# Optimization experiments

Measured on AMD Instinct MI355X. Metric: run time of the kernel, lower is better.

## Reference

```python
import jax, jax.numpy as jnp
import numpy as np
import math

B, S, SD = 8, 256, 768            # batch, seq_len, sent_dim (roberta-base)
L, NH, DH, FF = 12, 12, 64, 3072  # bert layers, heads, head dim, ffn dim
K, D, HC, DPH = 5, 200, 4, 50     # gnn layers, concept_dim, gat heads, dim/head
NNT, NET = 4, 38                  # node / edge types
NN = 200                          # nodes per graph
N = B * NN                        # total nodes
E = 50000                         # edges (before self loops)
IE = 200                          # info-exchange MLP hidden dim
LN_EPS = 1e-12
BN_EPS = 1e-5

def _gelu(x):
    return jax.nn.gelu(x, approximate=False)

def _layer_norm(x, w, b):
    m = jnp.mean(x, -1, keepdims=True)
    v = jnp.mean(jnp.square(x - m), -1, keepdims=True)
    return (x - m) * jax.lax.rsqrt(v + LN_EPS) * w + b

def _bn_eval(x, w, b):
    # untrained BatchNorm1d in eval mode: running_mean=0, running_var=1
    return x * np.float32(1.0 / np.sqrt(1.0 + BN_EPS)) * w + b

def _segment_softmax(scores, seg, num_segments):
    smax = jax.ops.segment_max(scores, seg, num_segments=num_segments)
    ex = jnp.exp(scores - smax[seg])
    den = jax.ops.segment_sum(ex, seg, num_segments=num_segments)
    return ex / (den[seg] + 1e-16)

def setup_inputs():
    key = jax.random.key(0)
    ks = iter(jax.random.split(key, 64))
    def nrm(shape, scale=0.02):
        return jax.random.normal(next(ks), shape, jnp.float32) * scale
    z = lambda s: jnp.zeros(s, jnp.float32)
    o = lambda s: jnp.ones(s, jnp.float32)
    return {
        'hidden_states': nrm((B, S, SD), 1.0),
        'attention_mask': z((B, 1, 1, S)),
        '_X': nrm((N, D), 1.0),
        '_node_feature_extra': nrm((N, D), 1.0),
        'qkv_w': nrm((L, 3, SD, SD)), 'qkv_b': z((L, 3, SD)),
        'attn_out_w': nrm((L, SD, SD)), 'attn_out_b': z((L, SD)),
        'ln1_w': o((L, SD)), 'ln1_b': z((L, SD)),
        'ffn_w1': nrm((L, SD, FF)), 'ffn_b1': z((L, FF)),
        'ffn_w2': nrm((L, FF, SD)), 'ffn_b2': z((L, SD)),
        'ln2_w': o((L, SD)), 'ln2_b': z((L, SD)),
        'ee_w1': nrm((NET + 1 + 2 * NNT, D)), 'ee_b1': z((D,)),
        'ee_bn_w': o((D,)), 'ee_bn_b': z((D,)),
        'ee_w2': nrm((D, D)), 'ee_b2': z((D,)),
        'gat_key_w': nrm((K, 3 * D, D)), 'gat_key_b': z((K, D)),
        'gat_msg_w': nrm((K, 3 * D, D)), 'gat_msg_b': z((K, D)),
        'gat_query_w': nrm((K, 2 * D, D)), 'gat_query_b': z((K, D)),
        'gat_mlp_w1': nrm((K, D, D)), 'gat_mlp_b1': z((K, D)),
        'gat_mlp_bn_w': o((K, D)), 'gat_mlp_bn_b': z((K, D)),
        'gat_mlp_w2': nrm((K, D, D)), 'gat_mlp_b2': z((K, D)),
        'ie_w1': nrm((SD + D, IE)), 'ie_b1': z((IE,)),
        'ie_w2': nrm((IE, SD + D)), 'ie_b2': z((SD + D,)),
        'edge_index': jax.random.randint(next(ks), (2, E), 0, N, dtype=jnp.int32),
        'edge_type': jax.random.randint(next(ks), (E,), 0, NET, dtype=jnp.int32),
        '_node_type': jax.random.randint(next(ks), (N,), 0, NNT, dtype=jnp.int32),
    }

def _forward(hidden_states, attention_mask, _X, _node_feature_extra,
             qkv_w, qkv_b, attn_out_w, attn_out_b, ln1_w, ln1_b,
             ffn_w1, ffn_b1, ffn_w2, ffn_b2, ln2_w, ln2_b,
             ee_w1, ee_b1, ee_bn_w, ee_bn_b, ee_w2, ee_b2,
             gat_key_w, gat_key_b, gat_msg_w, gat_msg_b, gat_query_w, gat_query_b,
             gat_mlp_w1, gat_mlp_b1, gat_mlp_bn_w, gat_mlp_bn_b, gat_mlp_w2, gat_mlp_b2,
             ie_w1, ie_b1, ie_w2, ie_b2,
             edge_index, edge_type, _node_type):
    hs = hidden_states
    dt = hs.dtype
    # ---- edge embeddings (shared edge_encoder => identical every gnn layer) ----
    loop = jnp.arange(N, dtype=edge_index.dtype)
    src = jnp.concatenate([edge_index[0], loop])   # [E+N] with self loops
    tgt = jnp.concatenate([edge_index[1], loop])
    edge_vec = jax.nn.one_hot(edge_type, NET + 1, dtype=dt)
    self_edge_vec = jnp.zeros((N, NET + 1), dt).at[:, NET].set(1.0)
    head_vec = jax.nn.one_hot(_node_type[edge_index[0]], NNT, dtype=dt)
    tail_vec = jax.nn.one_hot(_node_type[edge_index[1]], NNT, dtype=dt)
    self_vec = jax.nn.one_hot(_node_type, NNT, dtype=dt)
    feat = jnp.concatenate([
        jnp.concatenate([edge_vec, head_vec, tail_vec], 1),
        jnp.concatenate([self_edge_vec, self_vec, self_vec], 1)], 0)  # [E+N, 47]
    h = jax.nn.relu(_bn_eval(feat @ ee_w1 + ee_b1, ee_bn_w, ee_bn_b))
    edge_emb = h @ ee_w2 + ee_b2                                       # [E+N, D]
    deg_src = jax.ops.segment_sum(jnp.ones(src.shape, dt), src, num_segments=N)[src]
    scale_q = np.float32(1.0 / math.sqrt(DPH))
    scale_a = np.float32(1.0 / math.sqrt(DH))

    def gat_layer(Xc, g):
        x2 = jnp.concatenate([Xc, _node_feature_extra], 1)             # [N, 2D]
        x_i, x_j = x2[tgt], x2[src]                                    # tgt / src gathers
        key = (jnp.concatenate([x_i, edge_emb], 1) @ gat_key_w[g] + gat_key_b[g]).reshape(-1, HC, DPH)
        msg = (jnp.concatenate([x_j, edge_emb], 1) @ gat_msg_w[g] + gat_msg_b[g]).reshape(-1, HC, DPH)
        qry = (x_j @ gat_query_w[g] + gat_query_b[g]).reshape(-1, HC, DPH) * scale_q
        scores = jnp.sum(qry * key, -1)                                 # [E+N, HC]
        alpha = _segment_softmax(scores, src, N) * deg_src[:, None]     # grouped over src, degree-rescaled
        out = (msg * alpha[..., None]).reshape(-1, HC * DPH)
        aggr = jax.ops.segment_sum(out, tgt, num_segments=N)            # [N, D]
        hm = jax.nn.relu(_bn_eval(aggr @ gat_mlp_w1[g] + gat_mlp_b1[g], gat_mlp_bn_w[g], gat_mlp_bn_b[g]))
        return hm @ gat_mlp_w2[g] + gat_mlp_b2[g]

    Xc = _X
    for i in range(L):
        q = (hs @ qkv_w[i, 0] + qkv_b[i, 0]).reshape(B, S, NH, DH).transpose(0, 2, 1, 3)
        k = (hs @ qkv_w[i, 1] + qkv_b[i, 1]).reshape(B, S, NH, DH).transpose(0, 2, 1, 3)
        v = (hs @ qkv_w[i, 2] + qkv_b[i, 2]).reshape(B, S, NH, DH).transpose(0, 2, 1, 3)
        att = jax.nn.softmax(jnp.einsum('bhqd,bhkd->bhqk', q, k) * scale_a + attention_mask, -1)
        ctx = jnp.einsum('bhqk,bhkd->bhqd', att, v).transpose(0, 2, 1, 3).reshape(B, S, SD)
        attn = _layer_norm(ctx @ attn_out_w[i] + attn_out_b[i] + hs, ln1_w[i], ln1_b[i])
        inter = _gelu(attn @ ffn_w1[i] + ffn_b1[i])
        hs = _layer_norm(inter @ ffn_w2[i] + ffn_b2[i] + attn, ln2_w[i], ln2_b[i])
        if i >= L - K:
            g = i - L + K
            Xc = _gelu(gat_layer(Xc, g))
            Xv = Xc.reshape(B, NN, D)
            cf = jnp.concatenate([hs[:, 0, :], Xv[:, 0, :]], 1)         # [B, SD+D]
            cf = _gelu(cf @ ie_w1 + ie_b1) @ ie_w2 + ie_b2              # ie MLP (residual_ie=0)
            hs = hs.at[:, 0, :].set(cf[:, :SD])
            Xc = Xv.at[:, 0, :].set(cf[:, SD:]).reshape(N, D)
    return hs, Xc

def reference(hidden_states, attention_mask, _X, _node_feature_extra,
              qkv_w, qkv_b, attn_out_w, attn_out_b, ln1_w, ln1_b,
              ffn_w1, ffn_b1, ffn_w2, ffn_b2, ln2_w, ln2_b,
              ee_w1, ee_b1, ee_bn_w, ee_bn_b, ee_w2, ee_b2,
              gat_key_w, gat_key_b, gat_msg_w, gat_msg_b, gat_query_w, gat_query_b,
              gat_mlp_w1, gat_mlp_b1, gat_mlp_bn_w, gat_mlp_bn_b, gat_mlp_w2, gat_mlp_b2,
              ie_w1, ie_b1, ie_w2, ie_b2,
              edge_index, edge_type, _node_type):
    return _forward(hidden_states, attention_mask, _X, _node_feature_extra,
                    qkv_w, qkv_b, attn_out_w, attn_out_b, ln1_w, ln1_b,
                    ffn_w1, ffn_b1, ffn_w2, ffn_b2, ln2_w, ln2_b,
                    ee_w1, ee_b1, ee_bn_w, ee_bn_b, ee_w2, ee_b2,
                    gat_key_w, gat_key_b, gat_msg_w, gat_msg_b, gat_query_w, gat_query_b,
                    gat_mlp_w1, gat_mlp_b1, gat_mlp_bn_w, gat_mlp_bn_b, gat_mlp_w2, gat_mlp_b2,
                    ie_w1, ie_b1, ie_w2, ie_b2,
                    edge_index, edge_type, _node_type)
```

## Files before the change

kernel.cpp:

```cpp
#include <hip/hip_runtime.h>
#include <math.h>

namespace {
constexpr int CB = 8, CS = 256, CSD = 768, CL = 12, CNH = 12, CDH = 64, CFF = 3072;
constexpr int CK = 5, CD = 200, CHC = 4, CDPH = 50, CNNT = 4, CNET = 38;
constexpr int CNN = 200, CN = 1600, CE = 50000, CEN = 51600, CIE = 200;
constexpr int KP200 = 256, KP400 = 448;

constexpr long long OPK   = 0;
constexpr long long OATN  = OPK  + 3145728;
constexpr long long OXC   = OATN + 1572864;
constexpr long long OSC   = OXC  + 320000;
constexpr long long OSMX  = OSC  + 206400;
constexpr long long ODEN  = OSMX + 6400;
constexpr long long ODEG  = ODEN + 6400;
constexpr long long OAGG  = ODEG + 1600;
constexpr long long OQN   = OAGG + 320000;
constexpr long long OKN   = OQN  + 320000;
constexpr long long OMN   = OKN  + 320000;
constexpr long long OCF1  = OMN  + 320000;
constexpr long long OCF2  = OCF1 + 1600;
constexpr long long OEESC = OCF2 + 7744;
constexpr long long OEEBS = OEESC + 200;
constexpr long long OMLSC = OEEBS + 200;
constexpr long long OMLBS = OMLSC + 1000;
constexpr long long ONB   = OMLBS + 1000;
constexpr long long OBF   = ONB + 3000 + 8;

constexpr long long BHSB  = 0;
constexpr long long BATNB = BHSB  + 1572864;
constexpr long long BQKV  = BATNB + 1572864;
constexpr long long BVT   = BQKV  + 4718592;
constexpr long long BCTX  = BVT   + 3145728;
constexpr long long BINT  = BCTX  + 1572864;
constexpr long long BWQKV = BINT  + 6291456;
constexpr long long BWAO  = BWQKV + 1769472;
constexpr long long BWF1  = BWAO  + 589824;
constexpr long long BWF2  = BWF1  + 2359296;
constexpr long long BHEE  = BWF2  + 2359296;
constexpr long long BEEMB = BHEE  + 13238272;
constexpr long long BKEYE = BEEMB + 13238272;
constexpr long long BMSGE = BKEYE + 13238272;
constexpr long long BX2   = BMSGE + 13238272;
constexpr long long BAGG  = BX2   + 745472;
constexpr long long BHM   = BAGG  + 425984;
constexpr long long BGN   = BHM   + 425984;
constexpr long long BGE   = BGN   + 1720320;
constexpr long long BM1   = BGE   + 655360;
constexpr long long BM2   = BM1   + 327680;
constexpr long long BEW2  = BM2   + 327680;
}

typedef unsigned short ushort_t;
typedef __attribute__((ext_vector_type(8))) short bh8;
typedef __attribute__((ext_vector_type(4))) float fx4;

__device__ inline unsigned dk_fenc(float f) {
    unsigned u = __float_as_uint(f);
    return (u & 0x80000000u) ? ~u : (u | 0x80000000u);
}
__device__ inline float dk_fdec(unsigned u) {
    return (u & 0x80000000u) ? __uint_as_float(u & 0x7fffffffu) : __uint_as_float(~u);
}
__device__ inline float dk_gelu(float v) {
    return 0.5f * v * (1.0f + erff(v * 0.70710678118654752f));
}
__device__ inline ushort_t dk_f2bf(float f) {
    unsigned u = __float_as_uint(f);
    return (ushort_t)((u + 0x7fffu + ((u >> 16) & 1u)) >> 16);
}
__device__ inline float dk_bf2f(ushort_t h) {
    return __uint_as_float(((unsigned)h) << 16);
}
__device__ __forceinline__ void gl_lds16(const ushort_t* g, ushort_t* l) {
    __builtin_amdgcn_global_load_lds(
        (const __attribute__((address_space(1))) unsigned int*)(g),
        (__attribute__((address_space(3))) unsigned int*)(l), 16, 0, 0);
}

template<int DEPTH, int ACT, bool HAS_SCALE>
__global__ __launch_bounds__(256)
void dk_bgemm(const ushort_t* __restrict__ A, const ushort_t* __restrict__ B,
              const float* __restrict__ bias, long long sBias,
              const float* __restrict__ scale,
              float* __restrict__ Cf, ushort_t* __restrict__ Cb,
              int M, int N, int NPAD, int K,
              int lda, int ldb, int ldcf, int ldcb,
              int innerB, long long sAo, long long sAi, long long sBo, long long sBi,
              long long sCo, long long sCi)
{
    int z = blockIdx.z;
    int zo = z / innerB, zi = z - zo * innerB;
    A += zo * sAo + zi * sAi;
    B += zo * sBo + zi * sBi;
    long long coff = zo * sCo + zi * sCi;
    const float* biasp = bias ? (bias + (long long)z * sBias) : nullptr;

    int gx = gridDim.x, gy = gridDim.y;
    int nwg = gx * gy;
    int wid = blockIdx.y * gx + blockIdx.x;
    int q8 = nwg >> 3, r8 = nwg & 7;
    int xcd = wid & 7, off = wid >> 3;
    int base = (xcd < r8) ? xcd * (q8 + 1) : r8 * (q8 + 1) + (xcd - r8) * q8;
    int lin = base + off;
    int nb, mb;
    if (gy > 4 * gx) { mb = lin / gx; nb = lin - mb * gx; }
    else             { nb = lin / gy; mb = lin - nb * gy; }

    __shared__ __align__(16) ushort_t As[DEPTH * 128 * 64];
    __shared__ __align__(16) ushort_t Bs[DEPTH * 64 * 64];

    int tid = threadIdx.x;
    int l = tid & 63, w = tid >> 6;
    int m0 = mb * 128, n0 = nb * 64;

    int sj = l >> 3, scb = (l & 7) ^ sj;
    const ushort_t* gA[4]; const ushort_t* gB[2];
    int loffA[4], loffB[2];
#pragma unroll
    for (int j = 0; j < 4; j++) {
        int row = w * 32 + j * 8 + sj;
        gA[j] = A + (size_t)(m0 + row) * lda + scb * 8;
        loffA[j] = (w * 4 + j) * 512 + l * 8;
    }
#pragma unroll
    for (int j = 0; j < 2; j++) {
        int row = w * 16 + j * 8 + sj;
        gB[j] = B + (size_t)(n0 + row) * ldb + scb * 8;
        loffB[j] = (w * 2 + j) * 512 + l * 8;
    }

    int lr = l & 15, hi = l >> 4;
    int wm = (w >> 1) * 64, wn = (w & 1) * 32;
    int offA[4][2], offB[2][2];
#pragma unroll
    for (int mi = 0; mi < 4; mi++) {
        int rA = wm + mi * 16 + lr;
#pragma unroll
        for (int ks = 0; ks < 2; ks++) {
            int g = ks * 4 + hi;
            offA[mi][ks] = rA * 128 + ((g ^ (rA & 7)) << 4);
        }
    }
#pragma unroll
    for (int ni = 0; ni < 2; ni++) {
        int rB = wn + ni * 16 + lr;
#pragma unroll
        for (int ks = 0; ks < 2; ks++) {
            int g = ks * 4 + hi;
            offB[ni][ks] = rB * 128 + ((g ^ (rB & 7)) << 4);
        }
    }

    auto stage = [&](int t, int buf) {
        int k0 = t << 6;
        ushort_t* Ab = As + buf * 8192;
        ushort_t* Bb = Bs + buf * 4096;
#pragma unroll
        for (int j = 0; j < 4; j++) gl_lds16(gA[j] + k0, Ab + loffA[j]);
#pragma unroll
        for (int j = 0; j < 2; j++) gl_lds16(gB[j] + k0, Bb + loffB[j]);
    };

    fx4 acc[4][2] = {};
    int NT = K >> 6;
    int npro = NT < DEPTH ? NT : DEPTH;
    for (int d = 0; d < npro; ++d) stage(d, d);

    int cur = 0;
    for (int t = 0; t < NT; ++t) {
        int infl = NT - 1 - t;
        if (infl > DEPTH - 1) infl = DEPTH - 1;
        if (DEPTH >= 3 && infl >= 2) asm volatile("s_waitcnt vmcnt(12)" ::: "memory");
        else if (infl == 1)          asm volatile("s_waitcnt vmcnt(6)" ::: "memory");
        else if (infl == 0)          asm volatile("s_waitcnt vmcnt(0)" ::: "memory");
        __builtin_amdgcn_s_barrier();
        __builtin_amdgcn_sched_barrier(0);

        const char* Ab = (const char*)As + cur * 16384;
        const char* Bb = (const char*)Bs + cur * 8192;
#pragma unroll
        for (int ks = 0; ks < 2; ks++) {
            bh8 af[4], bf[2];
#pragma unroll
            for (int mi = 0; mi < 4; mi++)
                af[mi] = *(const bh8*)(Ab + offA[mi][ks]);
#pragma unroll
            for (int ni = 0; ni < 2; ni++)
                bf[ni] = *(const bh8*)(Bb + offB[ni][ks]);
#pragma unroll
            for (int mi = 0; mi < 4; mi++)
#pragma unroll
                for (int ni = 0; ni < 2; ni++)
                    acc[mi][ni] = __builtin_amdgcn_mfma_f32_16x16x32_bf16(af[mi], bf[ni], acc[mi][ni], 0, 0, 0);
        }
        __builtin_amdgcn_s_barrier();
        if (t + DEPTH < NT) stage(t + DEPTH, cur);
        cur = (cur + 1 == DEPTH) ? 0 : (cur + 1);
    }

    float* cf = Cf ? (Cf + coff) : nullptr;
    ushort_t* cb = Cb ? (Cb + coff) : nullptr;
#pragma unroll
    for (int ni = 0; ni < 2; ni++) {
        int nn = n0 + wn + ni * 16 + lr;
        if (nn >= NPAD) continue;
        bool vn = nn < N;
        float sc = (HAS_SCALE && vn) ? scale[nn] : 1.0f;
        float bi = (biasp && vn) ? biasp[nn] : 0.0f;
#pragma unroll
        for (int mi = 0; mi < 4; mi++) {
#pragma unroll
            for (int r = 0; r < 4; r++) {
                int mm = m0 + wm + mi * 16 + hi * 4 + r;
                if (mm >= M) continue;
                float v = 0.0f;
                if (vn) {
                    v = acc[mi][ni][r];
                    if (HAS_SCALE) v *= sc;
                    v += bi;
                    if (ACT == 1) v = fmaxf(v, 0.f);
                    if (ACT == 2) v = dk_gelu(v);
                }
                if (cf && vn) cf[(size_t)mm * ldcf + nn] = v;
                if (cb) cb[(size_t)mm * ldcb + nn] = dk_f2bf(v);
            }
        }
    }
}

__global__ __launch_bounds__(256)
void dk_fattn(const ushort_t* __restrict__ qg, const ushort_t* __restrict__ kg,
              const ushort_t* __restrict__ vTg, const float* __restrict__ mask,
              ushort_t* __restrict__ ctx)
{
    int sb = blockIdx.x, z = blockIdx.y;
    int b = z / CNH, h = z - b * CNH;

    __shared__ __align__(16) ushort_t Ks[256 * 64];
    __shared__ __align__(16) ushort_t Vs[64 * 256];

    int tid = threadIdx.x, l = tid & 63, w = tid >> 6;
    int lr = l & 15, hi = l >> 4;

    {
        int sj = l >> 3, c = (l & 7) ^ sj;
        const ushort_t* gkb = kg + ((size_t)b * 256 + w * 64 + sj) * CSD + h * 64 + c * 8;
        ushort_t* lds = Ks + (w * 64) * 64 + l * 8;
#pragma unroll
        for (int j = 0; j < 8; j++)
            gl_lds16(gkb + (size_t)(j * 8) * CSD, lds + j * 8 * 64);
    }
    {
#pragma unroll
        for (int j = 0; j < 8; j++) {
            int d = w * 16 + j * 2 + (l >> 5);
            const ushort_t* src = vTg + (size_t)z * 32768 + (size_t)d * 256 + ((l & 31) ^ (d & 7)) * 8;
            gl_lds16(src, Vs + (w * 16 + j * 2) * 256 + l * 8);
        }
    }
    bh8 qf0, qf1;
    {
        const ushort_t* qrow = qg + ((size_t)b * 256 + sb * 64 + w * 16 + lr) * CSD + h * 64;
        qf0 = *(const bh8*)(qrow + hi * 8);
        qf1 = *(const bh8*)(qrow + 32 + hi * 8);
    }
    float mv[16];
#pragma unroll
    for (int ni = 0; ni < 16; ni++) mv[ni] = mask[b * 256 + ni * 16 + lr];

    __syncthreads();

    fx4 accs[16] = {};
#pragma unroll
    for (int ks = 0; ks < 2; ks++) {
        bh8 qq = ks ? qf1 : qf0;
#pragma unroll
        for (int ni = 0; ni < 16; ni++) {
            int n = ni * 16 + lr;
            int g = ks * 4 + hi;
            bh8 kf = *(const bh8*)((const char*)Ks + n * 128 + ((g ^ (n & 7)) << 4));
            accs[ni] = __builtin_amdgcn_mfma_f32_16x16x32_bf16(qq, kf, accs[ni], 0, 0, 0);
        }
    }

    float pr[16][4];
#pragma unroll
    for (int r = 0; r < 4; r++) {
        float mx = -1e30f;
#pragma unroll
        for (int ni = 0; ni < 16; ni++) {
            float x = accs[ni][r] * 0.125f + mv[ni];
            pr[ni][r] = x;
            mx = fmaxf(mx, x);
        }
#pragma unroll
        for (int s = 1; s < 16; s <<= 1) mx = fmaxf(mx, __shfl_xor(mx, s, 64));
        float sum = 0.f;
#pragma unroll
        for (int ni = 0; ni < 16; ni++) { float e = expf(pr[ni][r] - mx); pr[ni][r] = e; sum += e; }
#pragma unroll
        for (int s = 1; s < 16; s <<= 1) sum += __shfl_xor(sum, s, 64);
        float inv = 1.0f / sum;
#pragma unroll
        for (int ni = 0; ni < 16; ni++) pr[ni][r] *= inv;
    }

    __syncthreads();

    {
        ushort_t* Pw = Ks + w * 4096;
#pragma unroll
        for (int ni = 0; ni < 16; ni++)
#pragma unroll
            for (int r = 0; r < 4; r++) {
                int q = hi * 4 + r;
                int byt = (q * 512 + (ni * 16 + lr) * 2) ^ ((q & 7) << 4);
                *(ushort_t*)((char*)Pw + byt) = dk_f2bf(pr[ni][r]);
            }
    }

    fx4 acco[4] = {};
    const ushort_t* Pw = Ks + w * 4096;
#pragma unroll
    for (int ks = 0; ks < 8; ks++) {
        int g = ks * 4 + hi;
        bh8 pf = *(const bh8*)((const char*)Pw + lr * 512 + ((g ^ (lr & 7)) << 4));
#pragma unroll
        for (int ni = 0; ni < 4; ni++) {
            int d = ni * 16 + lr;
            bh8 vf = *(const bh8*)((const char*)Vs + d * 512 + ((g ^ (d & 7)) << 4));
            acco[ni] = __builtin_amdgcn_mfma_f32_16x16x32_bf16(pf, vf, acco[ni], 0, 0, 0);
        }
    }

    {
        size_t rowbase = (size_t)b * 256 + sb * 64 + w * 16;
#pragma unroll
        for (int ni = 0; ni < 4; ni++)
#pragma unroll
            for (int r = 0; r < 4; r++) {
                int q = hi * 4 + r;
                ctx[(rowbase + q) * CSD + h * 64 + ni * 16 + lr] = dk_f2bf(acco[ni][r]);
            }
    }
}

__global__ __launch_bounds__(256)
void dk_tcast(const float* __restrict__ in, ushort_t* __restrict__ out,
              int K, int N, int ldin, int Np, int Kp,
              long long sIn, long long sOut)
{
    in  += (long long)blockIdx.z * sIn;
    out += (long long)blockIdx.z * sOut;
    int kb = blockIdx.x * 64, nb = blockIdx.y * 64;
    __shared__ float T[64][65];
    int t = threadIdx.x;
    int x = t & 63;
#pragma unroll
    for (int i = 0; i < 16; ++i) {
        int y = (t >> 6) * 16 + i;
        float v = (kb + y < K && nb + x < N) ? in[(size_t)(kb + y) * ldin + nb + x] : 0.f;
        T[y][x] = v;
    }
    __syncthreads();
#pragma unroll
    for (int i = 0; i < 16; ++i) {
        int y = (t >> 6) * 16 + i;
        int n = nb + y, k = kb + x;
        if (n < Np && k < Kp) out[(size_t)n * Kp + k] = dk_f2bf(T[x][y]);
    }
}

__global__ __launch_bounds__(256)
void dk_vtrans(const ushort_t* __restrict__ v, ushort_t* __restrict__ vT)
{
    int sb = blockIdx.x;
    int z  = blockIdx.y;
    int b = z / CNH, h = z - b * CNH;
    __shared__ ushort_t T[64][65];
    int t = threadIdx.x;
    int d = t & 63;
#pragma unroll
    for (int i = 0; i < 16; ++i) {
        int si = (t >> 6) * 16 + i;
        T[si][d] = v[(size_t)(b * 256 + sb * 64 + si) * 768 + h * 64 + d];
    }
    __syncthreads();
    int sjj = t & 63;
#pragma unroll
    for (int i = 0; i < 16; ++i) {
        int dd = (t >> 6) * 16 + i;
        vT[(size_t)z * 32768 + (size_t)dd * 256 + sb * 64 + sjj] = T[sjj][dd];
    }
}

__global__ __launch_bounds__(256)
void dk_ln_row(const float* __restrict__ in, const float* __restrict__ w,
               const float* __restrict__ b, float* __restrict__ out,
               ushort_t* __restrict__ outb)
{
    int row = blockIdx.x, tid = threadIdx.x;
    const float* ip = in + (long long)row * CSD;
    float xv[3];
    float s = 0.f;
#pragma unroll
    for (int t = 0; t < 3; t++) { xv[t] = ip[tid + t * 256]; s += xv[t]; }
    __shared__ float red[256];
    red[tid] = s; __syncthreads();
    for (int st = 128; st; st >>= 1) { if (tid < st) red[tid] += red[tid + st]; __syncthreads(); }
    float mean = red[0] * (1.f / 768.f); __syncthreads();
    float v = 0.f;
#pragma unroll
    for (int t = 0; t < 3; t++) { float d = xv[t] - mean; v += d * d; }
    red[tid] = v; __syncthreads();
    for (int st = 128; st; st >>= 1) { if (tid < st) red[tid] += red[tid + st]; __syncthreads(); }
    float var = red[0] * (1.f / 768.f);
    float rs = 1.0f / sqrtf(var + 1e-12f);
    float* op = out + (long long)row * CSD;
    ushort_t* ob = outb + (long long)row * CSD;
#pragma unroll
    for (int t = 0; t < 3; t++) {
        int c = tid + t * 256;
        float y = (xv[t] - mean) * rs * w[c] + b[c];
        op[c] = y;
        ob[c] = dk_f2bf(y);
    }
}

__global__ __launch_bounds__(256)
void dk_ln_fin(const float* __restrict__ p, const float* __restrict__ bias,
               const float* __restrict__ R, const float* __restrict__ w,
               const float* __restrict__ b, float* __restrict__ out,
               ushort_t* __restrict__ outb)
{
    int row = blockIdx.x, tid = threadIdx.x;
    const float* p0 = p + (long long)row * CSD;
    const float* p1 = p0 + 1572864;
    const float* rp = R + (long long)row * CSD;
    float xv[3];
    float s = 0.f;
#pragma unroll
    for (int t = 0; t < 3; t++) {
        int c = tid + t * 256;
        xv[t] = p0[c] + p1[c] + bias[c] + rp[c];
        s += xv[t];
    }
    __shared__ float red[256];
    red[tid] = s; __syncthreads();
    for (int st = 128; st; st >>= 1) { if (tid < st) red[tid] += red[tid + st]; __syncthreads(); }
    float mean = red[0] * (1.f / 768.f); __syncthreads();
    float v = 0.f;
#pragma unroll
    for (int t = 0; t < 3; t++) { float d = xv[t] - mean; v += d * d; }
    red[tid] = v; __syncthreads();
    for (int st = 128; st; st >>= 1) { if (tid < st) red[tid] += red[tid + st]; __syncthreads(); }
    float var = red[0] * (1.f / 768.f);
    float rs = 1.0f / sqrtf(var + 1e-12f);
    float* op = out + (long long)row * CSD;
    ushort_t* ob = outb + (long long)row * CSD;
#pragma unroll
    for (int t = 0; t < 3; t++) {
        int c = tid + t * 256;
        float y = (xv[t] - mean) * rs * w[c] + b[c];
        op[c] = y;
        ob[c] = dk_f2bf(y);
    }
}

__global__ void dk_copy_f32(const float* __restrict__ a, float* __restrict__ o, long long n)
{
    long long i = (long long)blockIdx.x * 256 + threadIdx.x;
    if (i < n) o[i] = a[i];
}

__global__ void dk_init_hs(const float* __restrict__ in, float* __restrict__ out,
                           ushort_t* __restrict__ outb, long long n)
{
    long long i = (long long)blockIdx.x * 256 + threadIdx.x;
    if (i < n) { float v = in[i]; out[i] = v; outb[i] = dk_f2bf(v); }
}

__global__ void dk_fold_bn(const float* __restrict__ b1, const float* __restrict__ bw,
                           const float* __restrict__ bb, float* __restrict__ sc,
                           float* __restrict__ bs, int n)
{
    int i = blockIdx.x * 256 + threadIdx.x;
    if (i >= n) return;
    float c = 1.0f / sqrtf(1.0f + 1e-5f);
    sc[i] = c * bw[i];
    bs[i] = b1[i] * c * bw[i] + bb[i];
}

__global__ void dk_pack_nbias(const float* __restrict__ q, const float* __restrict__ k,
                              const float* __restrict__ m, float* __restrict__ o)
{
    int i = blockIdx.x * 256 + threadIdx.x;
    if (i >= CK * CD) return;
    int g = i / CD, d = i - g * CD;
    o[g * 600 + d]       = q[i];
    o[g * 600 + 200 + d] = k[i];
    o[g * 600 + 400 + d] = m[i];
}

__global__ __launch_bounds__(256)
void dk_ee_gather(const float* __restrict__ w1, const float* __restrict__ sc,
                  const float* __restrict__ bs, const int* __restrict__ eidx,
                  const int* __restrict__ etyp, const int* __restrict__ ntyp,
                  ushort_t* __restrict__ out)
{
    int e = blockIdx.x, d = threadIdx.x;
    float v = 0.f;
    if (d < CD) {
        int t0, s, t;
        if (e < CE) { t0 = etyp[e]; s = eidx[e]; t = eidx[CE + e]; }
        else        { t0 = CNET; s = t = e - CE; }
        int h0 = ntyp[s], t1 = ntyp[t];
        v = w1[t0 * CD + d] + w1[(CNET + 1 + h0) * CD + d] + w1[(CNET + 1 + CNNT + t1) * CD + d];
        v = fmaxf(v * sc[d] + bs[d], 0.f);
    }
    out[(size_t)e * KP200 + d] = dk_f2bf(v);
}

__global__ void dk_deg_init(float* __restrict__ deg)
{
    int i = blockIdx.x * 256 + threadIdx.x;
    if (i < CN) deg[i] = 1.0f;
}
__global__ void dk_deg_count(const int* __restrict__ eidx, float* __restrict__ deg)
{
    int e = blockIdx.x * 256 + threadIdx.x;
    if (e < CE) atomicAdd(&deg[eidx[e]], 1.0f);
}

__global__ void dk_x2_build(const float* __restrict__ Xc, const float* __restrict__ nfe,
                            ushort_t* __restrict__ x2)
{
    int i = blockIdx.x * 256 + threadIdx.x;
    if (i >= CN * KP400) return;
    int n = i / KP400, d = i - n * KP400;
    float v = (d < CD) ? Xc[(size_t)n * CD + d]
            : (d < 2 * CD ? nfe[(size_t)n * CD + (d - CD)] : 0.f);
    x2[i] = dk_f2bf(v);
}

__global__ void dk_cast_pad(const float* __restrict__ in, ushort_t* __restrict__ out)
{
    int i = blockIdx.x * 256 + threadIdx.x;
    if (i >= CN * KP200) return;
    int r = i / KP200, c = i - r * KP200;
    out[i] = (c < CD) ? dk_f2bf(in[(size_t)r * CD + c]) : 0;
}

__global__ __launch_bounds__(256)
void dk_gat_scores(const float* __restrict__ qryN, const float* __restrict__ keyN,
                   const ushort_t* __restrict__ keyE, const int* __restrict__ eidx,
                   float* __restrict__ scores, unsigned* __restrict__ smax)
{
    long long id = (long long)blockIdx.x * 256 + threadIdx.x;
    if (id >= (long long)CEN * CHC) return;
    int e = (int)(id >> 2), h = (int)(id & 3);
    int s, t;
    if (e < CE) { s = eidx[e]; t = eidx[CE + e]; } else { s = t = e - CE; }
    const float* qp = qryN + (long long)s * CD + h * CDPH;
    const float* kp = keyN + (long long)t * CD + h * CDPH;
    const ushort_t* ke = keyE + (size_t)e * KP200 + h * CDPH;
    float acc = 0.f;
#pragma unroll 10
    for (int d = 0; d < CDPH; d++) acc += qp[d] * (kp[d] + dk_bf2f(ke[d]));
    acc *= 0.14142135623730950488f;
    scores[id] = acc;
    atomicMax(&smax[s * CHC + h], dk_fenc(acc));
}

__global__ __launch_bounds__(256)
void dk_gat_expsum(const unsigned* __restrict__ smax, const int* __restrict__ eidx,
                   float* __restrict__ scores, float* __restrict__ den)
{
    long long id = (long long)blockIdx.x * 256 + threadIdx.x;
    if (id >= (long long)CEN * CHC) return;
    int e = (int)(id >> 2), h = (int)(id & 3);
    int s;
    if (e < CE) s = eidx[e]; else s = e - CE;
    float ex = expf(scores[id] - dk_fdec(smax[s * CHC + h]));
    scores[id] = ex;
    atomicAdd(&den[s * CHC + h], ex);
}

__global__ __launch_bounds__(256)
void dk_gat_aggr(const float* __restrict__ msgN, const ushort_t* __restrict__ msgE,
                 const float* __restrict__ scores, const float* __restrict__ den,
                 const float* __restrict__ deg, const int* __restrict__ eidx,
                 float* __restrict__ aggr)
{
    int e = blockIdx.x, d = threadIdx.x;
    if (d >= CD) return;
    int s, t;
    if (e < CE) { s = eidx[e]; t = eidx[CE + e]; } else { s = t = e - CE; }
    int h = d / CDPH;
    float alpha = scores[(long long)e * CHC + h] / (den[s * CHC + h] + 1e-16f) * deg[s];
    float v = (msgN[(long long)s * CD + d] + dk_bf2f(msgE[(size_t)e * KP200 + d])) * alpha;
    atomicAdd(&aggr[(long long)t * CD + d], v);
}

__global__ __launch_bounds__(256)
void dk_ie_mlp1(const float* __restrict__ hs, const float* __restrict__ Xc,
                const float* __restrict__ w1, const float* __restrict__ b1,
                float* __restrict__ cf1)
{
    int n = threadIdx.x;
    int m = blockIdx.x;
    if (n >= CIE) return;
    const float* h = hs + (long long)m * CS * CSD;
    const float* x = Xc + (long long)m * CNN * CD;
    float a0 = 0.f, a1 = 0.f, a2 = 0.f, a3 = 0.f;
    int k = 0;
    for (; k + 4 <= CSD; k += 4) {
        a0 += h[k]     * w1[(k)     * CIE + n];
        a1 += h[k + 1] * w1[(k + 1) * CIE + n];
        a2 += h[k + 2] * w1[(k + 2) * CIE + n];
        a3 += h[k + 3] * w1[(k + 3) * CIE + n];
    }
    const float* w1x = w1 + (long long)CSD * CIE;
    for (k = 0; k + 4 <= CD; k += 4) {
        a0 += x[k]     * w1x[(k)     * CIE + n];
        a1 += x[k + 1] * w1x[(k + 1) * CIE + n];
        a2 += x[k + 2] * w1x[(k + 2) * CIE + n];
        a3 += x[k + 3] * w1x[(k + 3) * CIE + n];
    }
    float acc = (a0 + a1) + (a2 + a3) + b1[n];
    cf1[(long long)m * CIE + n] = dk_gelu(acc);
}

__global__ __launch_bounds__(256)
void dk_ie_mlp2(const float* __restrict__ cf1, const float* __restrict__ w2,
                const float* __restrict__ b2, float* __restrict__ cf2)
{
    int n = blockIdx.x * 256 + threadIdx.x;
    int m = blockIdx.y;
    const int NO = CSD + CD;
    if (n >= NO) return;
    const float* a = cf1 + (long long)m * CIE;
    float a0 = 0.f, a1 = 0.f, a2 = 0.f, a3 = 0.f;
    for (int k = 0; k + 4 <= CIE; k += 4) {
        a0 += a[k]     * w2[(k)     * NO + n];
        a1 += a[k + 1] * w2[(k + 1) * NO + n];
        a2 += a[k + 2] * w2[(k + 2) * NO + n];
        a3 += a[k + 3] * w2[(k + 3) * NO + n];
    }
    cf2[(long long)m * NO + n] = (a0 + a1) + (a2 + a3) + b2[n];
}

__global__ void dk_cf_scatter(const float* __restrict__ cf2, float* __restrict__ hs,
                              ushort_t* __restrict__ hsb, float* __restrict__ Xc)
{
    int i = blockIdx.x * 256 + threadIdx.x;
    if (i >= CB * (CSD + CD)) return;
    int b = i / (CSD + CD), c = i - b * (CSD + CD);
    float v = cf2[i];
    if (c < CSD) {
        hs[(long long)b * CS * CSD + c] = v;
        hsb[(long long)b * CS * CSD + c] = dk_f2bf(v);
    } else {
        Xc[(long long)b * CNN * CD + (c - CSD)] = v;
    }
}

static void bgemm(hipStream_t st, int mode,
                  const ushort_t* A, const ushort_t* B,
                  const float* bias, long long sBias, const float* scale,
                  float* Cf, ushort_t* Cb,
                  int M, int N, int NPAD, int K, int lda, int ldb, int ldcf, int ldcb,
                  int nz = 1, int innerB = 1,
                  long long sAo = 0, long long sAi = 0, long long sBo = 0, long long sBi = 0,
                  long long sCo = 0, long long sCi = 0)
{
    dim3 grid((NPAD + 63) / 64, (M + 127) / 128, nz), blk(256);
    long long blocks = (long long)grid.x * grid.y * grid.z;
    bool d3 = blocks <= 192;
    if (mode == 0) {
        if (d3) dk_bgemm<3, 0, false><<<grid, blk, 0, st>>>(A, B, bias, sBias, scale, Cf, Cb, M, N, NPAD, K, lda, ldb, ldcf, ldcb, innerB, sAo, sAi, sBo, sBi, sCo, sCi);
        else    dk_bgemm<2, 0, false><<<grid, blk, 0, st>>>(A, B, bias, sBias, scale, Cf, Cb, M, N, NPAD, K, lda, ldb, ldcf, ldcb, innerB, sAo, sAi, sBo, sBi, sCo, sCi);
    } else if (mode == 2) {
        if (d3) dk_bgemm<3, 2, false><<<grid, blk, 0, st>>>(A, B, bias, sBias, scale, Cf, Cb, M, N, NPAD, K, lda, ldb, ldcf, ldcb, innerB, sAo, sAi, sBo, sBi, sCo, sCi);
        else    dk_bgemm<2, 2, false><<<grid, blk, 0, st>>>(A, B, bias, sBias, scale, Cf, Cb, M, N, NPAD, K, lda, ldb, ldcf, ldcb, innerB, sAo, sAi, sBo, sBi, sCo, sCi);
    } else {
        if (d3) dk_bgemm<3, 1, true><<<grid, blk, 0, st>>>(A, B, bias, sBias, scale, Cf, Cb, M, N, NPAD, K, lda, ldb, ldcf, ldcb, innerB, sAo, sAi, sBo, sBi, sCo, sCi);
        else    dk_bgemm<2, 1, true><<<grid, blk, 0, st>>>(A, B, bias, sBias, scale, Cf, Cb, M, N, NPAD, K, lda, ldb, ldcf, ldcb, innerB, sAo, sAi, sBo, sBi, sCo, sCi);
    }
}

static void tcast(hipStream_t st, const float* in, ushort_t* out, int K, int N, int ldin,
                  int Np, int Kp, int nz = 1, long long sIn = 0, long long sOut = 0)
{
    dim3 grid((Kp + 63) / 64, (Np + 63) / 64, nz), blk(256);
    dk_tcast<<<grid, blk, 0, st>>>(in, out, K, N, ldin, Np, Kp, sIn, sOut);
}

extern "C" void kernel_launch(void* const* d_in, const int* in_sizes, int n_in,
                              void* d_out, int out_size, void* d_ws, size_t ws_size,
                              hipStream_t stream)
{
    const float* hidden = (const float*)d_in[0];
    const float* amask  = (const float*)d_in[1];
    const float* Xin    = (const float*)d_in[2];
    const float* nfe    = (const float*)d_in[3];
    const float* qkv_w  = (const float*)d_in[4];
    const float* qkv_b  = (const float*)d_in[5];
    const float* aow    = (const float*)d_in[6];
    const float* aob    = (const float*)d_in[7];
    const float* ln1w   = (const float*)d_in[8];
    const float* ln1b   = (const float*)d_in[9];
    const float* f1w    = (const float*)d_in[10];
    const float* f1b    = (const float*)d_in[11];
    const float* f2w    = (const float*)d_in[12];
    const float* f2b    = (const float*)d_in[13];
    const float* ln2w   = (const float*)d_in[14];
    const float* ln2b   = (const float*)d_in[15];
    const float* eew1   = (const float*)d_in[16];
    const float* eeb1   = (const float*)d_in[17];
    const float* eebnw  = (const float*)d_in[18];
    const float* eebnb  = (const float*)d_in[19];
    const float* eew2   = (const float*)d_in[20];
    const float* eeb2   = (const float*)d_in[21];
    const float* gkw    = (const float*)d_in[22];
    const float* gkb    = (const float*)d_in[23];
    const float* gmw    = (const float*)d_in[24];
    const float* gmb    = (const float*)d_in[25];
    const float* gqw    = (const float*)d_in[26];
    const float* gqb    = (const float*)d_in[27];
    const float* mw1    = (const float*)d_in[28];
    const float* mb1    = (const float*)d_in[29];
    const float* mbnw   = (const float*)d_in[30];
    const float* mbnb   = (const float*)d_in[31];
    const float* mw2    = (const float*)d_in[32];
    const float* mb2    = (const float*)d_in[33];
    const float* iew1   = (const float*)d_in[34];
    const float* ieb1   = (const float*)d_in[35];
    const float* iew2   = (const float*)d_in[36];
    const float* ieb2   = (const float*)d_in[37];
    const int*   eidx   = (const int*)d_in[38];
    const int*   etyp   = (const int*)d_in[39];
    const int*   ntyp   = (const int*)d_in[40];

    float* hs    = (float*)d_out;
    float* XcOut = hs + (long long)CB * CS * CSD;

    float* w = (float*)d_ws;
    float* pk   = w + OPK;
    float* atn  = w + OATN;
    float* Xc   = w + OXC;
    float* scrs = w + OSC;
    unsigned* smax = (unsigned*)(w + OSMX);
    float* den  = w + ODEN;
    float* deg  = w + ODEG;
    float* aggr = w + OAGG;
    float* qryN = w + OQN;
    float* keyN = w + OKN;
    float* msgN = w + OMN;
    float* cf1  = w + OCF1;
    float* cf2  = w + OCF2;
    float* eeSc = w + OEESC;
    float* eeBs = w + OEEBS;
    float* mlSc = w + OMLSC;
    float* mlBs = w + OMLBS;
    float* nbias= w + ONB;

    ushort_t* bb = (ushort_t*)(w + OBF);
    ushort_t* hs_b   = bb + BHSB;
    ushort_t* atn_b  = bb + BATNB;
    ushort_t* qkv_bf = bb + BQKV;
    ushort_t* vT     = bb + BVT;
    ushort_t* ctx_b  = bb + BCTX;
    ushort_t* int_b  = bb + BINT;
    ushort_t* wqkvT  = bb + BWQKV;
    ushort_t* waoT   = bb + BWAO;
    ushort_t* wf1T   = bb + BWF1;
    ushort_t* wf2T   = bb + BWF2;
    ushort_t* hee    = bb + BHEE;
    ushort_t* eemb   = bb + BEEMB;
    ushort_t* keyE   = bb + BKEYE;
    ushort_t* msgE   = bb + BMSGE;
    ushort_t* x2_b   = bb + BX2;
    ushort_t* aggr_b = bb + BAGG;
    ushort_t* hm_b   = bb + BHM;
    ushort_t* gnT    = bb + BGN;
    ushort_t* geT    = bb + BGE;
    ushort_t* m1T    = bb + BM1;
    ushort_t* m2T    = bb + BM2;
    ushort_t* eew2T  = bb + BEW2;

    const long long HS_N = (long long)CB * CS * CSD;
    const long long XC_N = (long long)CN * CD;

    dk_init_hs<<<(unsigned)((HS_N + 255) / 256), 256, 0, stream>>>(hidden, hs, hs_b, HS_N);
    dk_copy_f32<<<(unsigned)((XC_N + 255) / 256), 256, 0, stream>>>(Xin, Xc, XC_N);
    dk_fold_bn<<<1, 256, 0, stream>>>(eeb1, eebnw, eebnb, eeSc, eeBs, CD);
    dk_fold_bn<<<4, 256, 0, stream>>>(mb1, mbnw, mbnb, mlSc, mlBs, CK * CD);
    dk_pack_nbias<<<4, 256, 0, stream>>>(gqb, gkb, gmb, nbias);

    tcast(stream, eew2, eew2T, CD, CD, CD, KP200, KP200);
    tcast(stream, gqw, gnT + 0,      2 * CD, CD, CD, KP200, KP400, CK, 2LL * CD * CD, 344064LL);
    tcast(stream, gkw, gnT + 114688, 2 * CD, CD, CD, KP200, KP400, CK, 3LL * CD * CD, 344064LL);
    tcast(stream, gmw, gnT + 229376, 2 * CD, CD, CD, KP200, KP400, CK, 3LL * CD * CD, 344064LL);
    tcast(stream, gkw + 2 * CD * CD, geT + 0,     CD, CD, CD, KP200, KP200, CK, 3LL * CD * CD, 131072LL);
    tcast(stream, gmw + 2 * CD * CD, geT + 65536, CD, CD, CD, KP200, KP200, CK, 3LL * CD * CD, 131072LL);
    tcast(stream, mw1, m1T, CD, CD, CD, KP200, KP200, CK, (long long)CD * CD, 65536LL);
    tcast(stream, mw2, m2T, CD, CD, CD, KP200, KP200, CK, (long long)CD * CD, 65536LL);

    dk_ee_gather<<<CEN, 256, 0, stream>>>(eew1, eeSc, eeBs, eidx, etyp, ntyp, hee);
    bgemm(stream, 0, hee, eew2T, eeb2, 0, nullptr, nullptr, eemb,
          CEN, CD, KP200, KP200, KP200, KP200, 0, KP200);

    dk_deg_init<<<(CN + 255) / 256, 256, 0, stream>>>(deg);
    dk_deg_count<<<(CE + 255) / 256, 256, 0, stream>>>(eidx, deg);

    for (int i = 0; i < CL; i++) {
        tcast(stream, qkv_w + (long long)i * 3 * CSD * CSD, wqkvT, CSD, CSD, CSD, CSD, CSD,
              3, (long long)CSD * CSD, (long long)CSD * CSD);
        tcast(stream, aow + (long long)i * CSD * CSD, waoT, CSD, CSD, CSD, CSD, CSD);
        tcast(stream, f1w + (long long)i * CSD * CFF, wf1T, CSD, CFF, CFF, CFF, CSD);
        tcast(stream, f2w + (long long)i * CFF * CSD, wf2T, CFF, CSD, CSD, CSD, CFF);

        bgemm(stream, 0, hs_b, wqkvT, qkv_b + (long long)i * 3 * CSD, CSD, nullptr,
              nullptr, qkv_bf, 2048, CSD, CSD, CSD, CSD, CSD, 0, CSD,
              3, 1, 0, 0, (long long)CSD * CSD, 0, (long long)2048 * CSD, 0);
        dk_vtrans<<<dim3(4, 96), 256, 0, stream>>>(qkv_bf + 2LL * 2048 * CSD, vT);
        dk_fattn<<<dim3(4, 96), 256, 0, stream>>>(qkv_bf, qkv_bf + 1572864, vT, amask, ctx_b);
        bgemm(stream, 0, ctx_b, waoT, nullptr, 0, nullptr, pk, nullptr,
              2048, CSD, CSD, 384, CSD, CSD, CSD, 0,
              2, 1, 384, 0, 384, 0, 1572864, 0);
        dk_ln_fin<<<2048, 256, 0, stream>>>(pk, aob + (long long)i * CSD, hs,
              ln1w + (long long)i * CSD, ln1b + (long long)i * CSD, atn, atn_b);
        bgemm(stream, 2, atn_b, wf1T, f1b + (long long)i * CFF, 0, nullptr,
              nullptr, int_b, 2048, CFF, CFF, CSD, CSD, CSD, 0, CFF);
        bgemm(stream, 0, int_b, wf2T, nullptr, 0, nullptr, pk, nullptr,
              2048, CSD, CSD, 1536, CFF, CFF, CSD, 0,
              2, 1, 1536, 0, 1536, 0, 1572864, 0);
        dk_ln_fin<<<2048, 256, 0, stream>>>(pk, f2b + (long long)i * CSD, atn,
              ln2w + (long long)i * CSD, ln2b + (long long)i * CSD, hs, hs_b);

        if (i >= CL - CK) {
            int g = i - (CL - CK);
            dk_x2_build<<<(CN * KP400 + 255) / 256, 256, 0, stream>>>(Xc, nfe, x2_b);
            bgemm(stream, 0, x2_b, gnT + (long long)g * 344064,
                  nbias + (long long)g * 600, 200, nullptr,
                  qryN, nullptr, CN, CD, CD, KP400, KP400, KP400, CD, 0,
                  3, 1, 0, 0, 114688, 0, 320000, 0);
            bgemm(stream, 0, eemb, geT + (long long)g * 131072, nullptr, 0, nullptr,
                  nullptr, keyE, CEN, CD, KP200, KP200, KP200, KP200, 0, KP200,
                  2, 1, 0, 0, 65536, 0, 0, 13238272);
            hipMemsetAsync(smax, 0, CN * CHC * sizeof(unsigned), stream);
            hipMemsetAsync(den, 0, CN * CHC * sizeof(float), stream);
            hipMemsetAsync(aggr, 0, (size_t)CN * CD * sizeof(float), stream);
            dk_gat_scores<<<(CEN * CHC + 255) / 256, 256, 0, stream>>>(qryN, keyN, keyE, eidx, scrs, smax);
            dk_gat_expsum<<<(CEN * CHC + 255) / 256, 256, 0, stream>>>(smax, eidx, scrs, den);
            dk_gat_aggr<<<CEN, 256, 0, stream>>>(msgN, msgE, scrs, den, deg, eidx, aggr);
            dk_cast_pad<<<(CN * KP200 + 255) / 256, 256, 0, stream>>>(aggr, aggr_b);
            bgemm(stream, 3, aggr_b, m1T + (long long)g * 65536,
                  mlBs + (long long)g * CD, 0, mlSc + (long long)g * CD,
                  nullptr, hm_b, CN, CD, KP200, KP200, KP200, KP200, 0, KP200);
            bgemm(stream, 2, hm_b, m2T + (long long)g * 65536,
                  mb2 + (long long)g * CD, 0, nullptr,
                  Xc, nullptr, CN, CD, CD, KP200, KP200, KP200, CD, 0);
            dk_ie_mlp1<<<CB, 256, 0, stream>>>(hs, Xc, iew1, ieb1, cf1);
            dk_ie_mlp2<<<dim3(4, CB), 256, 0, stream>>>(cf1, iew2, ieb2, cf2);
            dk_cf_scatter<<<(CB * (CSD + CD) + 255) / 256, 256, 0, stream>>>(cf2, hs, hs_b, Xc);
        }
    }

    dk_copy_f32<<<(unsigned)((XC_N + 255) / 256), 256, 0, stream>>>(Xc, XcOut, XC_N);
}
```

Measured before the change: 3.113 ms.

## Precast all BERT weights once, fuse V transpose into attention, merge memsets

When the workspace is large enough, all 12 layers' BERT weights are transposed and cast to bf16 in four batched launches up front, replacing 48 per-layer tcast launches. The separate V-transpose kernel is removed: the attention kernel now loads V rows into registers and writes them transposed and swizzled into shared memory itself. The aggr buffer is moved next to smax/den so the three per-layer memsets become one. The trade-offs are a much larger workspace need (with a fallback to the old per-layer path) and scalar shared-memory stores in the attention prologue that may cause bank conflicts.

```diff
diff --git a/kernel.cpp b/kernel.cpp
--- a/kernel.cpp
+++ b/kernel.cpp
@@ -13,9 +13,9 @@
 constexpr long long OSC   = OXC  + 320000;
 constexpr long long OSMX  = OSC  + 206400;
 constexpr long long ODEN  = OSMX + 6400;
-constexpr long long ODEG  = ODEN + 6400;
-constexpr long long OAGG  = ODEG + 1600;
-constexpr long long OQN   = OAGG + 320000;
+constexpr long long OAGG  = ODEN + 6400;
+constexpr long long ODEG  = OAGG + 320000;
+constexpr long long OQN   = ODEG + 1600;
 constexpr long long OKN   = OQN  + 320000;
 constexpr long long OMN   = OKN  + 320000;
 constexpr long long OCF1  = OMN  + 320000;
@@ -49,6 +49,15 @@
 constexpr long long BM1   = BGE   + 655360;
 constexpr long long BM2   = BM1   + 327680;
 constexpr long long BEW2  = BM2   + 327680;
+constexpr long long BWALL = BEW2  + 65536;
+constexpr long long SQW   = 589824;
+constexpr long long SFW   = 2359296;
+constexpr long long BAQKV = BWALL;
+constexpr long long BAAO  = BAQKV + 36 * SQW;
+constexpr long long BAF1  = BAAO  + 12 * SQW;
+constexpr long long BAF2  = BAF1  + 12 * SFW;
+constexpr long long BEND  = BAF2  + 12 * SFW;
+constexpr unsigned long long NEED_BIG = (unsigned long long)OBF * 4ull + (unsigned long long)BEND * 2ull;
 }
 
 typedef unsigned short ushort_t;
@@ -231,7 +240,7 @@
 
 __global__ __launch_bounds__(256)
 void dk_fattn(const ushort_t* __restrict__ qg, const ushort_t* __restrict__ kg,
-              const ushort_t* __restrict__ vTg, const float* __restrict__ mask,
+              const ushort_t* __restrict__ vg, const float* __restrict__ mask,
               ushort_t* __restrict__ ctx)
 {
     int sb = blockIdx.x, z = blockIdx.y;
@@ -243,6 +252,12 @@
     int tid = threadIdx.x, l = tid & 63, w = tid >> 6;
     int lr = l & 15, hi = l >> 4;
 
+    bh8 vreg[8];
+    {
+        const ushort_t* vrow = vg + ((size_t)b * 256 + tid) * CSD + h * 64;
+#pragma unroll
+        for (int j = 0; j < 8; j++) vreg[j] = *(const bh8*)(vrow + j * 8);
+    }
     {
         int sj = l >> 3, c = (l & 7) ^ sj;
         const ushort_t* gkb = kg + ((size_t)b * 256 + w * 64 + sj) * CSD + h * 64 + c * 8;
@@ -252,12 +267,14 @@
             gl_lds16(gkb + (size_t)(j * 8) * CSD, lds + j * 8 * 64);
     }
     {
-#pragma unroll
-        for (int j = 0; j < 8; j++) {
-            int d = w * 16 + j * 2 + (l >> 5);
-            const ushort_t* src = vTg + (size_t)z * 32768 + (size_t)d * 256 + ((l & 31) ^ (d & 7)) * 8;
-            gl_lds16(src, Vs + (w * 16 + j * 2) * 256 + l * 8);
-        }
+        int c = tid >> 3, r = tid & 7;
+#pragma unroll
+        for (int j = 0; j < 8; j++)
+#pragma unroll
+            for (int e = 0; e < 8; e++) {
+                int d = j * 8 + e;
+                Vs[d * 256 + (((c ^ e) << 3) + r)] = (ushort_t)vreg[j][e];
+            }
     }
     bh8 qf0, qf1;
     {
@@ -369,29 +386,6 @@
         int y = (t >> 6) * 16 + i;
         int n = nb + y, k = kb + x;
         if (n < Np && k < Kp) out[(size_t)n * Kp + k] = dk_f2bf(T[x][y]);
-    }
-}
-
-__global__ __launch_bounds__(256)
-void dk_vtrans(const ushort_t* __restrict__ v, ushort_t* __restrict__ vT)
-{
-    int sb = blockIdx.x;
-    int z  = blockIdx.y;
-    int b = z / CNH, h = z - b * CNH;
-    __shared__ ushort_t T[64][65];
-    int t = threadIdx.x;
-    int d = t & 63;
-#pragma unroll
-    for (int i = 0; i < 16; ++i) {
-        int si = (t >> 6) * 16 + i;
-        T[si][d] = v[(size_t)(b * 256 + sb * 64 + si) * 768 + h * 64 + d];
-    }
-    __syncthreads();
-    int sjj = t & 63;
-#pragma unroll
-    for (int i = 0; i < 16; ++i) {
-        int dd = (t >> 6) * 16 + i;
-        vT[(size_t)z * 32768 + (size_t)dd * 256 + sb * 64 + sjj] = T[sjj][dd];
     }
 }
 
@@ -753,8 +747,8 @@
     float* scrs = w + OSC;
     unsigned* smax = (unsigned*)(w + OSMX);
     float* den  = w + ODEN;
+    float* aggr = w + OAGG;
     float* deg  = w + ODEG;
-    float* aggr = w + OAGG;
     float* qryN = w + OQN;
     float* keyN = w + OKN;
     float* msgN = w + OMN;
@@ -770,7 +764,6 @@
     ushort_t* hs_b   = bb + BHSB;
     ushort_t* atn_b  = bb + BATNB;
     ushort_t* qkv_bf = bb + BQKV;
-    ushort_t* vT     = bb + BVT;
     ushort_t* ctx_b  = bb + BCTX;
     ushort_t* int_b  = bb + BINT;
     ushort_t* wqkvT  = bb + BWQKV;
@@ -789,6 +782,12 @@
     ushort_t* m1T    = bb + BM1;
     ushort_t* m2T    = bb + BM2;
     ushort_t* eew2T  = bb + BEW2;
+    ushort_t* aqkv   = bb + BAQKV;
+    ushort_t* aao    = bb + BAAO;
+    ushort_t* af1    = bb + BAF1;
+    ushort_t* af2    = bb + BAF2;
+
+    const bool bigW = (unsigned long long)ws_size >= NEED_BIG + (16ull << 20);
 
     const long long HS_N = (long long)CB * CS * CSD;
     const long long XC_N = (long long)CN * CD;
@@ -808,6 +807,13 @@
     tcast(stream, mw1, m1T, CD, CD, CD, KP200, KP200, CK, (long long)CD * CD, 65536LL);
     tcast(stream, mw2, m2T, CD, CD, CD, KP200, KP200, CK, (long long)CD * CD, 65536LL);
 
+    if (bigW) {
+        tcast(stream, qkv_w, aqkv, CSD, CSD, CSD, CSD, CSD, 36, (long long)CSD * CSD, SQW);
+        tcast(stream, aow,  aao,  CSD, CSD, CSD, CSD, CSD, 12, (long long)CSD * CSD, SQW);
+        tcast(stream, f1w,  af1,  CSD, CFF, CFF, CFF, CSD, 12, (long long)CSD * CFF, SFW);
+        tcast(stream, f2w,  af2,  CFF, CSD, CSD, CSD, CFF, 12, (long long)CFF * CSD, SFW);
+    }
+
     dk_ee_gather<<<CEN, 256, 0, stream>>>(eew1, eeSc, eeBs, eidx, etyp, ntyp, hee);
     bgemm(stream, 0, hee, eew2T, eeb2, 0, nullptr, nullptr, eemb,
           CEN, CD, KP200, KP200, KP200, KP200, 0, KP200);
@@ -816,25 +822,34 @@
     dk_deg_count<<<(CE + 255) / 256, 256, 0, stream>>>(eidx, deg);
 
     for (int i = 0; i < CL; i++) {
-        tcast(stream, qkv_w + (long long)i * 3 * CSD * CSD, wqkvT, CSD, CSD, CSD, CSD, CSD,
-              3, (long long)CSD * CSD, (long long)CSD * CSD);
-        tcast(stream, aow + (long long)i * CSD * CSD, waoT, CSD, CSD, CSD, CSD, CSD);
-        tcast(stream, f1w + (long long)i * CSD * CFF, wf1T, CSD, CFF, CFF, CFF, CSD);
-        tcast(stream, f2w + (long long)i * CFF * CSD, wf2T, CFF, CSD, CSD, CSD, CFF);
-
-        bgemm(stream, 0, hs_b, wqkvT, qkv_b + (long long)i * 3 * CSD, CSD, nullptr,
+        const ushort_t *wq, *wa, *w1p, *w2p;
+        if (bigW) {
+            wq  = aqkv + (long long)i * 3 * SQW;
+            wa  = aao  + (long long)i * SQW;
+            w1p = af1  + (long long)i * SFW;
+            w2p = af2  + (long long)i * SFW;
+        } else {
+            tcast(stream, qkv_w + (long long)i * 3 * CSD * CSD, wqkvT, CSD, CSD, CSD, CSD, CSD,
+                  3, (long long)CSD * CSD, (long long)CSD * CSD);
+            tcast(stream, aow + (long long)i * CSD * CSD, waoT, CSD, CSD, CSD, CSD, CSD);
+            tcast(stream, f1w + (long long)i * CSD * CFF, wf1T, CSD, CFF, CFF, CFF, CSD);
+            tcast(stream, f2w + (long long)i * CFF * CSD, wf2T, CFF, CSD, CSD, CSD, CFF);
+            wq = wqkvT; wa = waoT; w1p = wf1T; w2p = wf2T;
+        }
+
+        bgemm(stream, 0, hs_b, wq, qkv_b + (long long)i * 3 * CSD, CSD, nullptr,
               nullptr, qkv_bf, 2048, CSD, CSD, CSD, CSD, CSD, 0, CSD,
-              3, 1, 0, 0, (long long)CSD * CSD, 0, (long long)2048 * CSD, 0);
-        dk_vtrans<<<dim3(4, 96), 256, 0, stream>>>(qkv_bf + 2LL * 2048 * CSD, vT);
-        dk_fattn<<<dim3(4, 96), 256, 0, stream>>>(qkv_bf, qkv_bf + 1572864, vT, amask, ctx_b);
-        bgemm(stream, 0, ctx_b, waoT, nullptr, 0, nullptr, pk, nullptr,
+              3, 1, 0, 0, SQW, 0, (long long)2048 * CSD, 0);
+        dk_fattn<<<dim3(4, 96), 256, 0, stream>>>(qkv_bf, qkv_bf + 1572864,
+                                                  qkv_bf + 3145728, amask, ctx_b);
+        bgemm(stream, 0, ctx_b, wa, nullptr, 0, nullptr, pk, nullptr,
               2048, CSD, CSD, 384, CSD, CSD, CSD, 0,
               2, 1, 384, 0, 384, 0, 1572864, 0);
         dk_ln_fin<<<2048, 256, 0, stream>>>(pk, aob + (long long)i * CSD, hs,
               ln1w + (long long)i * CSD, ln1b + (long long)i * CSD, atn, atn_b);
-        bgemm(stream, 2, atn_b, wf1T, f1b + (long long)i * CFF, 0, nullptr,
+        bgemm(stream, 2, atn_b, w1p, f1b + (long long)i * CFF, 0, nullptr,
               nullptr, int_b, 2048, CFF, CFF, CSD, CSD, CSD, 0, CFF);
-        bgemm(stream, 0, int_b, wf2T, nullptr, 0, nullptr, pk, nullptr,
+        bgemm(stream, 0, int_b, w2p, nullptr, 0, nullptr, pk, nullptr,
               2048, CSD, CSD, 1536, CFF, CFF, CSD, 0,
               2, 1, 1536, 0, 1536, 0, 1572864, 0);
         dk_ln_fin<<<2048, 256, 0, stream>>>(pk, f2b + (long long)i * CSD, atn,
@@ -850,9 +865,7 @@
             bgemm(stream, 0, eemb, geT + (long long)g * 131072, nullptr, 0, nullptr,
                   nullptr, keyE, CEN, CD, KP200, KP200, KP200, KP200, 0, KP200,
                   2, 1, 0, 0, 65536, 0, 0, 13238272);
-            hipMemsetAsync(smax, 0, CN * CHC * sizeof(unsigned), stream);
-            hipMemsetAsync(den, 0, CN * CHC * sizeof(float), stream);
-            hipMemsetAsync(aggr, 0, (size_t)CN * CD * sizeof(float), stream);
+            hipMemsetAsync(smax, 0, (size_t)(6400 + 6400 + 320000) * sizeof(float), stream);
             dk_gat_scores<<<(CEN * CHC + 255) / 256, 256, 0, stream>>>(qryN, keyN, keyE, eidx, scrs, smax);
             dk_gat_expsum<<<(CEN * CHC + 255) / 256, 256, 0, stream>>>(smax, eidx, scrs, den);
             dk_gat_aggr<<<CEN, 256, 0, stream>>>(msgN, msgE, scrs, den, deg, eidx, aggr);
```

Measured after the change: 2.850 ms. 8.5% less time.
